# Kernel optimization log

Hardware: AMD Instinct MI355X
Metric: run time of the kernel (lower is better)

The kernel has to match this reference:

```python
import jax, jax.numpy as jnp
import numpy as np

D_MODEL = 256
NUM_HEADS = 8
D_HEAD = D_MODEL // NUM_HEADS  # 32


def setup_inputs() -> dict:
    key = jax.random.key(0)
    ks = jax.random.split(key, 7)
    N, WH = 8, 2048
    s = 1.0 / np.sqrt(D_MODEL)
    return {
        "x": jax.random.normal(ks[0], (N, WH, D_MODEL), dtype=jnp.float32),
        "Wq": jax.random.normal(ks[1], (D_MODEL, D_MODEL), dtype=jnp.float32) * s,
        "bq": jnp.zeros((D_MODEL,), dtype=jnp.float32),
        "Wk": jax.random.normal(ks[2], (D_MODEL, D_MODEL), dtype=jnp.float32) * s,
        "bk": jnp.zeros((D_MODEL,), dtype=jnp.float32),
        "Wv": jax.random.normal(ks[3], (D_MODEL, D_MODEL), dtype=jnp.float32) * s,
        "bv": jnp.zeros((D_MODEL,), dtype=jnp.float32),
    }


def _mhsa(x, Wq, bq, Wk, bk, Wv, bv):
    N, WH, C = x.shape
    # QKV projections; reshape to (N, heads, WH, d_head)
    def split_heads(t):
        return t.reshape(N, WH, NUM_HEADS, D_HEAD).transpose(0, 2, 1, 3)
    Q = split_heads(x @ Wq + bq)
    K = split_heads(x @ Wk + bk)
    V = split_heads(x @ Wv + bv)
    # FAITHFUL to source: logits /= d_k**(-0.5)  ==  logits * sqrt(d_k)
    logits = jnp.einsum("nhqd,nhkd->nhqk", Q, K) * jnp.sqrt(jnp.float32(D_HEAD))
    attn = jax.nn.softmax(logits, axis=-1)  # dropout p=0.1 is identity in eval
    x_attn = jnp.einsum("nhqk,nhkd->nhqd", attn, V)
    x_attn = x_attn.transpose(0, 2, 1, 3).reshape(N, WH, C)
    # drop_path is identity in eval mode; residual add
    return x_attn + x


def reference(x, Wq, bq, Wk, bk, Wv, bv):
    return _mhsa(x, Wq, bq, Wk, bk, Wv, bv)
```

## Files before the change

kernel.cpp:

```cpp
#include <hip/hip_runtime.h>
#include <math.h>

#define WH 2048
#define DM 256
#define NHD 8
#define DH 32
#define NB 8

typedef __attribute__((ext_vector_type(8))) short short8;
typedef __attribute__((ext_vector_type(4))) short short4v;
typedef __attribute__((ext_vector_type(4))) float f32x4;

__device__ __forceinline__ unsigned short bf16_rn(float f) {
    unsigned u = __float_as_uint(f);
    return (unsigned short)((u + 0x8000u) >> 16);
}
__device__ __forceinline__ float bf16_to_f(unsigned short h) {
    return __uint_as_float(((unsigned)h) << 16);
}
__device__ __forceinline__ unsigned pack_bf16_rtz(float f1, float f0) {
    return __builtin_amdgcn_perm(__float_as_uint(f1), __float_as_uint(f0), 0x07060302);
}
__device__ __forceinline__ void glds16(const void* g, void* l) {
    __builtin_amdgcn_global_load_lds(
        (const __attribute__((address_space(1))) unsigned int*)g,
        (__attribute__((address_space(3))) unsigned int*)l, 16, 0, 0);
}

__global__ __launch_bounds__(256) void prep(
    const float* __restrict__ X,
    const float* __restrict__ Wq, const float* __restrict__ Wk, const float* __restrict__ Wv,
    unsigned short* __restrict__ Xhi, unsigned short* __restrict__ Xlo,
    unsigned short* __restrict__ WThi, unsigned short* __restrict__ WTlo)
{
    const int bid = blockIdx.x;
    if (bid < 2048) {
        const size_t i = ((size_t)bid * 256 + threadIdx.x) * 8;
        const int row = (int)(i >> 8);
        const int k   = (int)(i & 255);
        const size_t dst = ((size_t)(k >> 5) * 16384 + row) * 32 + (k & 31);
        float4 a = *(const float4*)&X[i];
        float4 b = *(const float4*)&X[i + 4];
        float v[8] = {a.x, a.y, a.z, a.w, b.x, b.y, b.z, b.w};
        short8 hi, lo;
        #pragma unroll
        for (int e = 0; e < 8; e++) {
            unsigned short hb = bf16_rn(v[e]);
            hi[e] = (short)hb;
            lo[e] = (short)bf16_rn(v[e] - bf16_to_f(hb));
        }
        *(short8*)&Xhi[dst] = hi;
        *(short8*)&Xlo[dst] = lo;
    } else {
        const int b2 = bid - 2048;
        const int z = b2 >> 4, xb = b2 & 15;
        const float* W = (z == 0) ? Wq : ((z == 1) ? Wk : Wv);
        const size_t zoff = (size_t)z * DM * DM;
        const int tg = xb * 256 + threadIdx.x;
        #pragma unroll
        for (int j = 0; j < 4; j++) {
            const int f = tg + j * 4096;
            const int k  = f >> 6;
            const int n0 = (f & 63) * 4;
            float4 v = *(const float4*)&W[(size_t)k * DM + n0];
            float vv[4] = {v.x, v.y, v.z, v.w};
            #pragma unroll
            for (int i = 0; i < 4; i++) {
                unsigned short hb = bf16_rn(vv[i]);
                const size_t dst = zoff + ((size_t)(k >> 5) * 256 + n0 + i) * 32 + (k & 31);
                WThi[dst] = hb;
                WTlo[dst] = bf16_rn(vv[i] - bf16_to_f(hb));
            }
        }
    }
}

__global__ __launch_bounds__(256, 3) void qkv_mfma(
    const unsigned short* __restrict__ Xhi, const unsigned short* __restrict__ Xlo,
    const unsigned short* __restrict__ WThi, const unsigned short* __restrict__ WTlo,
    const float* __restrict__ bq, const float* __restrict__ bk, const float* __restrict__ bv,
    unsigned short* __restrict__ Qhi, unsigned short* __restrict__ Qlo,
    unsigned short* __restrict__ KV)
{
    __shared__ __align__(16) unsigned short arena[16896];

    const int z = blockIdx.z;
    const float* bias = (z == 0) ? bq : ((z == 1) ? bk : bv);
    const size_t zoff = (size_t)z * DM * DM;

    const int tid  = threadIdx.x;
    const int w    = tid >> 6;
    const int lane = tid & 63;
    const int col  = lane & 15;
    const int quad = lane >> 4;
    const int wr = w >> 1, wc = w & 1;
    const int bm = blockIdx.x * 128;
    const int bn = blockIdx.y * 128;

    const int perm16 = (((lane & 3) ^ ((lane >> 3) & 3))) * 16;
    const char* glane; size_t kstr;
    if (w == 0)      { glane = (const char*)Xhi + (size_t)(bm + (lane >> 2)) * 64 + perm16; kstr = (size_t)16384 * 64; }
    else if (w == 1) { glane = (const char*)Xlo + (size_t)(bm + (lane >> 2)) * 64 + perm16; kstr = (size_t)16384 * 64; }
    else if (w == 2) { glane = (const char*)(WThi + zoff) + (size_t)(bn + (lane >> 2)) * 64 + perm16; kstr = 256 * 64; }
    else             { glane = (const char*)(WTlo + zoff) + (size_t)(bn + (lane >> 2)) * 64 + perm16; kstr = 256 * 64; }

    auto issue = [&](int kb) {
        const char* g0 = glane + (size_t)kb * kstr;
        unsigned short* l0 = &arena[w * 4096];
        #pragma unroll
        for (int g = 0; g < 8; g++)
            glds16(g0 + (size_t)g * 1024, l0 + g * 512);
    };

    f32x4 acc[4][4];
    #pragma unroll
    for (int mi = 0; mi < 4; mi++)
        #pragma unroll
        for (int ni = 0; ni < 4; ni++) acc[mi][ni] = (f32x4){0.f, 0.f, 0.f, 0.f};

    const int sw = (col >> 1) & 3;
    const int fO = (quad ^ sw) * 8;

    for (int kb = 0; kb < 8; kb++) {
        issue(kb);
        __syncthreads();

        short8 ah[4], al[4], bh[4], bl[4];
        #pragma unroll
        for (int mi = 0; mi < 4; mi++) {
            const int ro = (wr * 64 + mi * 16 + col) * 32 + fO;
            ah[mi] = *(const short8*)&arena[ro];
            al[mi] = *(const short8*)&arena[4096 + ro];
        }
        #pragma unroll
        for (int ni = 0; ni < 4; ni++) {
            const int no = (wc * 64 + ni * 16 + col) * 32 + fO;
            bh[ni] = *(const short8*)&arena[8192 + no];
            bl[ni] = *(const short8*)&arena[12288 + no];
        }
        #pragma unroll
        for (int mi = 0; mi < 4; mi++)
            #pragma unroll
            for (int ni = 0; ni < 4; ni++) {
                acc[mi][ni] = __builtin_amdgcn_mfma_f32_16x16x32_bf16(al[mi], bh[ni], acc[mi][ni], 0, 0, 0);
                acc[mi][ni] = __builtin_amdgcn_mfma_f32_16x16x32_bf16(ah[mi], bl[ni], acc[mi][ni], 0, 0, 0);
                acc[mi][ni] = __builtin_amdgcn_mfma_f32_16x16x32_bf16(ah[mi], bh[ni], acc[mi][ni], 0, 0, 0);
            }
        __syncthreads();
    }

    unsigned* Tp = (unsigned*)arena;
    const int n   = bm >> 11;
    const int wqb = bm & (WH - 1);
    const float qsc = (z == 0) ? 8.1611159f : 1.0f;

    #pragma unroll
    for (int p = 0; p < 2; p++) {
        if (wr == p) {
            #pragma unroll
            for (int mi = 0; mi < 4; mi++)
                #pragma unroll
                for (int ni = 0; ni < 4; ni++) {
                    const int lc = wc * 64 + ni * 16 + col;
                    const float bb = bias[bn + lc];
                    #pragma unroll
                    for (int r = 0; r < 4; r++) {
                        float v = (acc[mi][ni][r] + bb) * qsc;
                        unsigned short hb = bf16_rn(v);
                        unsigned short lb = bf16_rn(v - bf16_to_f(hb));
                        Tp[(mi * 16 + quad * 4 + r) * 132 + lc] =
                            (unsigned)hb | ((unsigned)lb << 16);
                    }
                }
        }
        __syncthreads();
        if (z == 2) {
            const int c = tid >> 1, half = tid & 1;
            const int coln = bn + c, h = coln >> 5, d = coln & 31;
            const int key0 = wqb + p * 64 + half * 32;
            const int t = key0 >> 6, k6 = key0 & 63;
            unsigned short* dst =
                &KV[(((size_t)(n * NHD + h) * 32 + t) * 6144) + 4096 + d * 64 + k6];
            unsigned hi[16];
            #pragma unroll
            for (int jj = 0; jj < 16; jj++) {
                unsigned u0 = Tp[(half * 32 + 2 * jj    ) * 132 + c];
                unsigned u1 = Tp[(half * 32 + 2 * jj + 1) * 132 + c];
                hi[jj] = __builtin_amdgcn_perm(u1, u0, 0x05040100);
            }
            #pragma unroll
            for (int s = 0; s < 4; s++)
                *(uint4*)&dst[s * 8] = make_uint4(hi[4*s], hi[4*s+1], hi[4*s+2], hi[4*s+3]);
        } else if (z == 1) {
            const int lr = tid >> 2, seg = tid & 3;
            const int h = (bn + seg * 32) >> 5;
            const int key = wqb + p * 64 + lr;
            const int t = key >> 6, k6 = key & 63;
            unsigned short* blobK =
                &KV[(((size_t)(n * NHD + h) * 32 + t) * 6144) + k6 * 32];
            #pragma unroll
            for (int s = 0; s < 4; s++) {
                unsigned u[8], hi[4], lo[4];
                *(uint4*)&u[0] = *(uint4*)&Tp[lr * 132 + seg * 32 + s * 8];
                *(uint4*)&u[4] = *(uint4*)&Tp[lr * 132 + seg * 32 + s * 8 + 4];
                #pragma unroll
                for (int jj = 0; jj < 4; jj++) {
                    hi[jj] = __builtin_amdgcn_perm(u[2*jj+1], u[2*jj], 0x05040100);
                    lo[jj] = __builtin_amdgcn_perm(u[2*jj+1], u[2*jj], 0x07060302);
                }
                *(uint4*)&blobK[s * 8]        = make_uint4(hi[0], hi[1], hi[2], hi[3]);
                *(uint4*)&blobK[2048 + s * 8] = make_uint4(lo[0], lo[1], lo[2], lo[3]);
            }
        } else {
            const int lr = tid >> 2, seg = tid & 3;
            const int h = (bn + seg * 32) >> 5;
            const size_t off = ((size_t)((n * NHD + h) * WH) + wqb + p * 64 + lr) * DH;
            #pragma unroll
            for (int s = 0; s < 4; s++) {
                unsigned u[8], hi[4], lo[4];
                *(uint4*)&u[0] = *(uint4*)&Tp[lr * 132 + seg * 32 + s * 8];
                *(uint4*)&u[4] = *(uint4*)&Tp[lr * 132 + seg * 32 + s * 8 + 4];
                #pragma unroll
                for (int jj = 0; jj < 4; jj++) {
                    hi[jj] = __builtin_amdgcn_perm(u[2*jj+1], u[2*jj], 0x05040100);
                    lo[jj] = __builtin_amdgcn_perm(u[2*jj+1], u[2*jj], 0x07060302);
                }
                *(uint4*)&Qhi[off + s * 8] = make_uint4(hi[0], hi[1], hi[2], hi[3]);
                *(uint4*)&Qlo[off + s * 8] = make_uint4(lo[0], lo[1], lo[2], lo[3]);
            }
        }
        __syncthreads();
    }
}

__global__ __launch_bounds__(256, 4) void attn(
    const unsigned short* __restrict__ Qhi, const unsigned short* __restrict__ Qlo,
    const unsigned short* __restrict__ KV,  const float* __restrict__ X,
    float* __restrict__ Out)
{
    __shared__ __align__(16) unsigned short B[2][6144];

    const int tid  = threadIdx.x;
    const int w    = tid >> 6;
    const int lane = tid & 63;
    const int col  = lane & 15;
    const int quad = lane >> 4;
    const int nh   = blockIdx.y;
    const int q0   = blockIdx.x * 128;
    const size_t qbase = (size_t)nh * WH * DH;
    const char* blob = (const char*)(KV + (size_t)nh * 196608);

    short8 qh[2], ql[2];
    #pragma unroll
    for (int f = 0; f < 2; f++) {
        const int qrow = q0 + f * 64 + w * 16 + col;
        qh[f] = *(const short8*)&Qhi[qbase + (size_t)qrow * DH + quad * 8];
        ql[f] = *(const short8*)&Qlo[qbase + (size_t)qrow * DH + quad * 8];
    }

    f32x4 o00 = {0.f,0.f,0.f,0.f}, o01 = {0.f,0.f,0.f,0.f};
    f32x4 o10 = {0.f,0.f,0.f,0.f}, o11 = {0.f,0.f,0.f,0.f};
    f32x4 la0 = {0.f,0.f,0.f,0.f}, la1 = {0.f,0.f,0.f,0.f};
    float mr0 = 0.f, mr1 = 0.f;

    const char* gseg[3];
    int loseg[3];
    #pragma unroll
    for (int j = 0; j < 3; j++) {
        const int s = w * 3 + j;
        int loff;
        if (s < 8) loff = (lane >> 2) * 64  + (((lane & 3) ^ ((lane >> 3) & 3)) << 4);
        else       loff = (lane >> 3) * 128 + (((lane & 7) ^ ((lane >> 3) & 7)) << 4);
        gseg[j] = blob + s * 1024 + loff;
        loseg[j] = s * 512;
    }

    auto issue = [&](int t, int b) {
        #pragma unroll
        for (int j = 0; j < 3; j++)
            glds16(gseg[j] + (size_t)t * 12288, &B[b][loseg[j]]);
    };

    const int sw = (col >> 1) & 3;
    const short4v ones = {(short)0x3F80, (short)0x3F80, (short)0x3F80, (short)0x3F80};

    auto body = [&](int b) {
        const unsigned short* Bp = &B[b][0];
        short8 kh[4], kl[4];
        #pragma unroll
        for (int kc = 0; kc < 4; kc++) {
            const int ro = (col + kc * 16) * 32 + (quad ^ sw) * 8;
            kh[kc] = *(const short8*)&Bp[ro];
            kl[kc] = *(const short8*)&Bp[2048 + ro];
        }
        short4v va[4][2];
        #pragma unroll
        for (int kc = 0; kc < 4; kc++) {
            const int cl = kc * 2 + (quad >> 1);
            const int co = ((cl ^ (col & 7)) << 3) + (quad & 1) * 4;
            va[kc][0] = *(const short4v*)&Bp[4096 + (col     ) * 64 + co];
            va[kc][1] = *(const short4v*)&Bp[4096 + (col + 16) * 64 + co];
        }
        #pragma unroll
        for (int f = 0; f < 2; f++) {
            f32x4 s[4];
            #pragma unroll
            for (int kc = 0; kc < 4; kc++) {
                f32x4 a = {0.f, 0.f, 0.f, 0.f};
                a = __builtin_amdgcn_mfma_f32_16x16x32_bf16(kh[kc], ql[f], a, 0, 0, 0);
                a = __builtin_amdgcn_mfma_f32_16x16x32_bf16(kl[kc], qh[f], a, 0, 0, 0);
                a = __builtin_amdgcn_mfma_f32_16x16x32_bf16(kh[kc], qh[f], a, 0, 0, 0);
                s[kc] = a;
            }
            float mx = s[0][0];
            #pragma unroll
            for (int kc = 0; kc < 4; kc++)
                #pragma unroll
                for (int r = 0; r < 4; r++) mx = fmaxf(mx, s[kc][r]);
            mx = fmaxf(mx, __shfl_xor(mx, 16));
            mx = fmaxf(mx, __shfl_xor(mx, 32));

            float& mrf = f ? mr1 : mr0;
            f32x4& a0 = f ? o10 : o00;
            f32x4& a1 = f ? o11 : o01;
            f32x4& la = f ? la1 : la0;
            const float mnew = fmaxf(mrf, mx);
            if (__any(mx > mrf)) {
                const float alpha = __builtin_amdgcn_exp2f(mrf - mnew);
                #pragma unroll
                for (int r = 0; r < 4; r++) { a0[r] *= alpha; a1[r] *= alpha; }
                la[0] *= alpha;
            }
            mrf = mnew;

            short4v pb[4];
            #pragma unroll
            for (int kc = 0; kc < 4; kc++) {
                const float p0 = __builtin_amdgcn_exp2f(s[kc][0] - mnew);
                const float p1 = __builtin_amdgcn_exp2f(s[kc][1] - mnew);
                const float p2 = __builtin_amdgcn_exp2f(s[kc][2] - mnew);
                const float p3 = __builtin_amdgcn_exp2f(s[kc][3] - mnew);
                union { short4v v; unsigned u[2]; } P;
                P.u[0] = pack_bf16_rtz(p1, p0);
                P.u[1] = pack_bf16_rtz(p3, p2);
                pb[kc] = P.v;
            }
            #pragma unroll
            for (int kc = 0; kc < 4; kc++) {
                a0 = __builtin_amdgcn_mfma_f32_16x16x16bf16_1k(va[kc][0], pb[kc], a0, 0, 0, 0);
                a1 = __builtin_amdgcn_mfma_f32_16x16x16bf16_1k(va[kc][1], pb[kc], a1, 0, 0, 0);
                la = __builtin_amdgcn_mfma_f32_16x16x16bf16_1k(ones,      pb[kc], la, 0, 0, 0);
            }
        }
    };

    issue(0, 0);
    __syncthreads();
    for (int t2 = 0; t2 < 16; t2++) {
        issue(2 * t2 + 1, 1);
        body(0);
        __syncthreads();
        if (t2 < 15) issue(2 * t2 + 2, 0);
        body(1);
        __syncthreads();
    }

    const int n = nh >> 3, h = nh & 7;
    #pragma unroll
    for (int f = 0; f < 2; f++) {
        const float inv = 1.f / (f ? la1[0] : la0[0]);
        const f32x4& a0 = f ? o10 : o00;
        const f32x4& a1 = f ? o11 : o01;
        const int qrow = q0 + f * 64 + w * 16 + col;
        const size_t a = ((size_t)n * WH + qrow) * DM + h * DH + quad * 4;
        float4 x0 = *(const float4*)&X[a];
        float4 y0;
        y0.x = a0[0] * inv + x0.x;
        y0.y = a0[1] * inv + x0.y;
        y0.z = a0[2] * inv + x0.z;
        y0.w = a0[3] * inv + x0.w;
        *(float4*)&Out[a] = y0;
        float4 x1 = *(const float4*)&X[a + 16];
        float4 y1;
        y1.x = a1[0] * inv + x1.x;
        y1.y = a1[1] * inv + x1.y;
        y1.z = a1[2] * inv + x1.z;
        y1.w = a1[3] * inv + x1.w;
        *(float4*)&Out[a + 16] = y1;
    }
}

extern "C" void kernel_launch(void* const* d_in, const int* in_sizes, int n_in,
                              void* d_out, int out_size, void* d_ws, size_t ws_size,
                              hipStream_t stream) {
    const float* x  = (const float*)d_in[0];
    const float* Wq = (const float*)d_in[1];
    const float* bq = (const float*)d_in[2];
    const float* Wk = (const float*)d_in[3];
    const float* bk = (const float*)d_in[4];
    const float* Wv = (const float*)d_in[5];
    const float* bv = (const float*)d_in[6];
    float* out = (float*)d_out;

    const size_t elems = (size_t)NB * WH * DM;
    unsigned short* Qhi  = (unsigned short*)d_ws;
    unsigned short* Qlo  = Qhi + elems;
    unsigned short* KV   = Qlo + elems;
    unsigned short* WThi = KV  + (size_t)64 * 32 * 6144;
    unsigned short* WTlo = WThi + (size_t)3 * DM * DM;

    unsigned short* Xhi = (unsigned short*)d_out;
    unsigned short* Xlo = Xhi + elems;

    prep<<<2096, 256, 0, stream>>>(x, Wq, Wk, Wv, Xhi, Xlo, WThi, WTlo);

    dim3 gg(128, 2, 3);
    qkv_mfma<<<gg, 256, 0, stream>>>(Xhi, Xlo, WThi, WTlo, bq, bk, bv,
                                     Qhi, Qlo, KV);

    dim3 ga(WH / 128, NB * NHD);
    attn<<<ga, 256, 0, stream>>>(Qhi, Qlo, KV, x, out);
}
```

Measured before the change: 205.0 us.

## Load QKV GEMM operands directly into registers with double buffering, dropping LDS staging

The QKV projection kernel no longer stages X and W tiles through shared memory with global_load_lds and barriers. Each wave now loads its bf16 hi/lo fragments straight from global memory into registers and prefetches the next k-block while running MFMAs on the current one. The launch-bounds occupancy hint is removed and shared memory shrinks to the transpose buffer. This removes the barriers and the LDS round-trip, but each wave now issues redundant global loads of the same data with a less coalesced pattern, and uses far more registers, which may lower occupancy.

```diff
diff --git a/kernel.cpp b/kernel.cpp
--- a/kernel.cpp
+++ b/kernel.cpp
@@ -75,14 +75,14 @@
     }
 }
 
-__global__ __launch_bounds__(256, 3) void qkv_mfma(
+__global__ __launch_bounds__(256) void qkv_mfma(
     const unsigned short* __restrict__ Xhi, const unsigned short* __restrict__ Xlo,
     const unsigned short* __restrict__ WThi, const unsigned short* __restrict__ WTlo,
     const float* __restrict__ bq, const float* __restrict__ bk, const float* __restrict__ bv,
     unsigned short* __restrict__ Qhi, unsigned short* __restrict__ Qlo,
     unsigned short* __restrict__ KV)
 {
-    __shared__ __align__(16) unsigned short arena[16896];
+    __shared__ __align__(16) unsigned Tp[64 * 132];
 
     const int z = blockIdx.z;
     const float* bias = (z == 0) ? bq : ((z == 1) ? bk : bv);
@@ -97,19 +97,20 @@
     const int bm = blockIdx.x * 128;
     const int bn = blockIdx.y * 128;
 
-    const int perm16 = (((lane & 3) ^ ((lane >> 3) & 3))) * 16;
-    const char* glane; size_t kstr;
-    if (w == 0)      { glane = (const char*)Xhi + (size_t)(bm + (lane >> 2)) * 64 + perm16; kstr = (size_t)16384 * 64; }
-    else if (w == 1) { glane = (const char*)Xlo + (size_t)(bm + (lane >> 2)) * 64 + perm16; kstr = (size_t)16384 * 64; }
-    else if (w == 2) { glane = (const char*)(WThi + zoff) + (size_t)(bn + (lane >> 2)) * 64 + perm16; kstr = 256 * 64; }
-    else             { glane = (const char*)(WTlo + zoff) + (size_t)(bn + (lane >> 2)) * 64 + perm16; kstr = 256 * 64; }
-
-    auto issue = [&](int kb) {
-        const char* g0 = glane + (size_t)kb * kstr;
-        unsigned short* l0 = &arena[w * 4096];
-        #pragma unroll
-        for (int g = 0; g < 8; g++)
-            glds16(g0 + (size_t)g * 1024, l0 + g * 512);
+    const size_t aoffs = (size_t)(bm + wr * 64 + col) * 32 + quad * 8;
+    const size_t boffs = zoff + (size_t)(bn + wc * 64 + col) * 32 + quad * 8;
+
+    short8 ah[2][4], al[2][4], bh[2][4], bl[2][4];
+    auto load = [&](int kb, int buf) {
+        #pragma unroll
+        for (int i = 0; i < 4; i++) {
+            const size_t ao = aoffs + (size_t)kb * 524288 + i * 512;
+            ah[buf][i] = *(const short8*)&Xhi[ao];
+            al[buf][i] = *(const short8*)&Xlo[ao];
+            const size_t bo = boffs + (size_t)kb * 8192 + i * 512;
+            bh[buf][i] = *(const short8*)&WThi[bo];
+            bl[buf][i] = *(const short8*)&WTlo[bo];
+        }
     };
 
     f32x4 acc[4][4];
@@ -118,38 +119,21 @@
         #pragma unroll
         for (int ni = 0; ni < 4; ni++) acc[mi][ni] = (f32x4){0.f, 0.f, 0.f, 0.f};
 
-    const int sw = (col >> 1) & 3;
-    const int fO = (quad ^ sw) * 8;
-
+    load(0, 0);
+    #pragma unroll
     for (int kb = 0; kb < 8; kb++) {
-        issue(kb);
-        __syncthreads();
-
-        short8 ah[4], al[4], bh[4], bl[4];
-        #pragma unroll
-        for (int mi = 0; mi < 4; mi++) {
-            const int ro = (wr * 64 + mi * 16 + col) * 32 + fO;
-            ah[mi] = *(const short8*)&arena[ro];
-            al[mi] = *(const short8*)&arena[4096 + ro];
-        }
-        #pragma unroll
-        for (int ni = 0; ni < 4; ni++) {
-            const int no = (wc * 64 + ni * 16 + col) * 32 + fO;
-            bh[ni] = *(const short8*)&arena[8192 + no];
-            bl[ni] = *(const short8*)&arena[12288 + no];
-        }
+        const int b = kb & 1;
+        if (kb < 7) load(kb + 1, b ^ 1);
         #pragma unroll
         for (int mi = 0; mi < 4; mi++)
             #pragma unroll
             for (int ni = 0; ni < 4; ni++) {
-                acc[mi][ni] = __builtin_amdgcn_mfma_f32_16x16x32_bf16(al[mi], bh[ni], acc[mi][ni], 0, 0, 0);
-                acc[mi][ni] = __builtin_amdgcn_mfma_f32_16x16x32_bf16(ah[mi], bl[ni], acc[mi][ni], 0, 0, 0);
-                acc[mi][ni] = __builtin_amdgcn_mfma_f32_16x16x32_bf16(ah[mi], bh[ni], acc[mi][ni], 0, 0, 0);
-            }
-        __syncthreads();
-    }
-
-    unsigned* Tp = (unsigned*)arena;
+                acc[mi][ni] = __builtin_amdgcn_mfma_f32_16x16x32_bf16(al[b][mi], bh[b][ni], acc[mi][ni], 0, 0, 0);
+                acc[mi][ni] = __builtin_amdgcn_mfma_f32_16x16x32_bf16(ah[b][mi], bl[b][ni], acc[mi][ni], 0, 0, 0);
+                acc[mi][ni] = __builtin_amdgcn_mfma_f32_16x16x32_bf16(ah[b][mi], bh[b][ni], acc[mi][ni], 0, 0, 0);
+            }
+    }
+
     const int n   = bm >> 11;
     const int wqb = bm & (WH - 1);
     const float qsc = (z == 0) ? 8.1611159f : 1.0f;
```

Measured after the change: 213.4 us. +4.1%, slower.
